# Kernel optimization log

Hardware: AMD Instinct MI355X
Metric: run time of the kernel (lower is better)

The kernel has to match this reference:

```python
import jax, jax.numpy as jnp
import numpy as np

IN_CH = 32
OUT_CH = 32
HIDDEN = 32  # edge/angle MLP hidden width


def setup_inputs() -> dict:
    key = jax.random.key(0)
    ks = jax.random.split(key, 13)
    N, E, A = 50000, 200000, 400000
    s = 0.1
    return {
        "x": jax.random.normal(ks[0], (N, IN_CH), dtype=jnp.float32),
        "edge_index": jax.random.randint(ks[1], (2, E), 0, N),
        "edge_attr": jax.random.uniform(ks[2], (E, 1), dtype=jnp.float32),
        "angle_index": jax.random.randint(ks[3], (3, A), 0, N),
        "angles": jax.random.uniform(ks[4], (A, 1), dtype=jnp.float32),
        # edge_mlp: Linear(1,32) -> ReLU -> Linear(32, in*out)
        "eW1": jax.random.normal(ks[5], (1, HIDDEN), dtype=jnp.float32) * s,
        "eb1": jax.random.normal(ks[6], (HIDDEN,), dtype=jnp.float32) * s,
        "eW2": jax.random.normal(ks[7], (HIDDEN, IN_CH * OUT_CH), dtype=jnp.float32) * s,
        "eb2": jax.random.normal(ks[8], (IN_CH * OUT_CH,), dtype=jnp.float32) * s,
        # angle_mlp: Linear(1,32) -> ReLU -> Linear(32, out)
        "aW1": jax.random.normal(ks[9], (1, HIDDEN), dtype=jnp.float32) * s,
        "ab1": jax.random.normal(ks[10], (HIDDEN,), dtype=jnp.float32) * s,
        "aW2": jax.random.normal(ks[11], (HIDDEN, OUT_CH), dtype=jnp.float32) * s,
        "ab2": jax.random.normal(ks[12], (OUT_CH,), dtype=jnp.float32) * s,
    }


def reference(x, edge_index, edge_attr, angle_index, angles,
              eW1, eb1, eW2, eb2, aW1, ab1, aW2, ab2):
    N = x.shape[0]
    row, col = edge_index[0], edge_index[1]
    # per-edge weight matrices from edge MLP: (E, in, out)
    h = jax.nn.relu(edge_attr @ eW1 + eb1)
    edge_w = (h @ eW2 + eb2).reshape(-1, IN_CH, OUT_CH)
    # gather source node features, apply per-edge matrix (bmm)
    msg = jnp.einsum('ei,eio->eo', x[col], edge_w)  # (E, out)
    agg = jax.ops.segment_sum(msg, row, num_segments=N)
    # angle branch: scatter angle features onto center node j
    j = angle_index[1]
    angle_feat = jax.nn.relu(angles @ aW1 + ab1) @ aW2 + ab2  # (A, out)
    agg = agg + jax.ops.segment_sum(angle_feat, j, num_segments=N)
    return agg
```

## Files before the change

### kernel.cpp

```cpp
#include <hip/hip_runtime.h>
#include <hip/hip_bf16.h>
#include <stdint.h>

#define IC 32
#define OC 32
#define HID 32

#define PBIN 16
#define TSH 44
#define TSCALE 1048576.0f

#define PBE 12

typedef __attribute__((ext_vector_type(8))) _Float16 half8;
typedef __attribute__((ext_vector_type(4))) float f32x4;
typedef unsigned long long u64;

static __device__ __forceinline__ _Float16 f2h(float f) { return (_Float16)f; }

__device__ __align__(16) _Float16 g_MK[PBE * 2 * 32 * 32];
__device__ float g_ekn[16];
__device__ float g_akn[16];
__device__ int   g_npc[2];

__global__ __launch_bounds__(256) void setup_kernel(
    const float* __restrict__ eW1, const float* __restrict__ eb1,
    const float* __restrict__ eW2, const float* __restrict__ eb2,
    const float* __restrict__ aW1, const float* __restrict__ ab1)
{
    __shared__ float ts_s[32];
    __shared__ int   rk_s[32];
    __shared__ int   re_s[32];
    const int tid = threadIdx.x;

    if (blockIdx.x == 0 && tid < 16) { g_ekn[tid] = 1e30f; g_akn[tid] = 1e30f; }

    if (tid < 32) {
        const int k = tid;
        const float w = eW1[k], b = eb1[k];
        const float ts = -b / w;
        const bool re = (w != 0.f) && (ts > 0.f) && (ts < 1.f);
        int rk = 0;
        for (int k2 = 0; k2 < 32; ++k2) {
            const float w2 = eW1[k2], b2 = eb1[k2];
            const float t2 = -b2 / w2;
            const bool re2 = (w2 != 0.f) && (t2 > 0.f) && (t2 < 1.f);
            rk += (re2 && (t2 < ts || (t2 == ts && k2 < k))) ? 1 : 0;
        }
        ts_s[k] = ts; rk_s[k] = rk; re_s[k] = re ? 1 : 0;
    }
    __syncthreads();

    if (blockIdx.x == 0) {
        if (tid < 32) {
            if (re_s[tid]) g_ekn[rk_s[tid]] = ts_s[tid];
            if (tid == 0) {
                int n = 0;
                for (int k = 0; k < 32; ++k) n += re_s[k];
                g_npc[0] = n + 1;
            }
        } else if (tid < 64) {
            const int k = tid - 32;
            const float w = aW1[k], b = ab1[k];
            const float ts = -b / w;
            const bool re = (w != 0.f) && (ts > 0.f) && (ts < 1.f);
            int rk = 0, nre = 0;
            for (int k2 = 0; k2 < 32; ++k2) {
                const float w2 = aW1[k2], b2 = ab1[k2];
                const float t2 = -b2 / w2;
                const bool re2 = (w2 != 0.f) && (t2 > 0.f) && (t2 < 1.f);
                nre += re2 ? 1 : 0;
                rk += (re2 && (t2 < ts || (t2 == ts && k2 < k))) ? 1 : 0;
            }
            if (re) g_akn[rk] = ts;
            if (k == 0) g_npc[1] = nre + 1;
        }
    }

    const int gid = blockIdx.x * blockDim.x + tid;
    if (gid < PBE * 2 * 32 * 32) {
        const int i   = gid & 31;
        const int o   = (gid >> 5) & 31;
        const int mat = (gid >> 10) & 1;
        const int cc  = gid >> 11;
        float acc = (mat == 0) ? eb2[i * 32 + o] : 0.f;
        for (int k = 0; k < 32; ++k) {
            const bool flip = re_s[k] && (rk_s[k] < cc);
            const float w = eW1[k], b = eb1[k];
            const bool on0 = b > 0.f;
            const bool on = (w > 0.f) ? (on0 || flip) : (on0 && !flip);
            if (on) acc = fmaf((mat == 0 ? b : w), eW2[k * 1024 + i * 32 + o], acc);
        }
        g_MK[((cc * 2 + mat) * 32 + o) * 32 + i] = (_Float16)acc;
    }
}

__global__ void zero_kernel(float* __restrict__ out, int n) {
    int i = (blockIdx.x * blockDim.x + threadIdx.x) * 4;
    if (i + 3 < n) {
        *(float4*)(out + i) = make_float4(0.f, 0.f, 0.f, 0.f);
    } else {
        for (int k = i; k < n; ++k) out[k] = 0.f;
    }
}

__global__ __launch_bounds__(256) void angle_scatter(
    const float* __restrict__ angles, const int* __restrict__ angle_index,
    u64* __restrict__ cells, int A)
{
    float kn[16];
#pragma unroll
    for (int j = 0; j < 16; ++j) kn[j] = g_akn[j];

    int i0 = blockIdx.x * blockDim.x + threadIdx.x;
    int stride = gridDim.x * blockDim.x;
    for (int a = i0; a < A; a += stride) {
        const float t = angles[a];
        const int j = angle_index[A + a];
        int cc = 0;
#pragma unroll
        for (int jj = 0; jj < 16; ++jj) cc += (t >= kn[jj]) ? 1 : 0;
        if ((unsigned)cc < (unsigned)PBIN) {
            const u64 enc = ((u64)1 << TSH) | (u64)(unsigned)(t * TSCALE);
            atomicAdd(cells + (size_t)j * PBIN + cc, enc);
        }
    }
}

__global__ __launch_bounds__(256) void angle_gather(
    float* __restrict__ out,
    const float* __restrict__ aW1, const float* __restrict__ ab1,
    const float* __restrict__ aW2, const float* __restrict__ ab2,
    int N)
{
    const int lane = threadIdx.x & 63;
    const int q    = lane >> 4;
    const int l15  = lane & 15;
    const int wib  = threadIdx.x >> 6;
    const int base = (blockIdx.x * 4 + wib) * 16;
    if (base >= N) return;

    float w1s[8], b1s[8];
    int c0 = 0, c1 = 0;
#pragma unroll
    for (int k = 0; k < HID; ++k) {
        const float w = aW1[k], b = ab1[k];
        const bool pos = w > 0.f;
        const bool f0 = pos ? (b > 0.f) : !(b > 0.f);
        const bool f1 = pos ? ((w + b) > 0.f) : !((w + b) > 0.f);
        c0 += f0 ? 1 : 0;
        c1 += f1 ? 1 : 0;
        if ((k >> 3) == q) { w1s[k & 7] = w; b1s[k & 7] = b; }
    }
    int npc = c1 - c0 + 1;
    if (npc > PBIN) npc = PBIN;

    half8 Bf0, Bf1;
#pragma unroll
    for (int j = 0; j < 8; ++j) {
        Bf0[j] = f2h(aW2[(q * 8 + j) * OC + l15]);
        Bf1[j] = f2h(aW2[(q * 8 + j) * OC + 16 + l15]);
    }
    const float bias0 = ab2[l15];
    const float bias1 = ab2[16 + l15];

    const int jn = base + l15;
    const bool vn = (jn < N);
    const u64* cj = (const u64*)out + (size_t)(vn ? jn : 0) * PBIN;
    float g[8] = {0.f, 0.f, 0.f, 0.f, 0.f, 0.f, 0.f, 0.f};
    float tot = 0.f;
    for (int cc = 0; cc < npc; ++cc) {
        const u64 v = vn ? cj[cc] : 0;
        if (v) {
            const float n  = (float)(unsigned)(v >> TSH);
            const float ts = (float)(v & (((u64)1 << TSH) - 1)) * (1.f / TSCALE);
            const float tb = ts / n;
#pragma unroll
            for (int k = 0; k < 8; ++k) {
                float h = fmaf(tb, w1s[k], b1s[k]);
                h = h > 0.f ? h : 0.f;
                g[k] = fmaf(n, h, g[k]);
            }
            tot += n;
        }
    }
    half8 a;
#pragma unroll
    for (int k = 0; k < 8; ++k) a[k] = f2h(g[k]);

    f32x4 acc0 = {0.f, 0.f, 0.f, 0.f};
    f32x4 acc1 = {0.f, 0.f, 0.f, 0.f};
    acc0 = __builtin_amdgcn_mfma_f32_16x16x32_f16(a, Bf0, acc0, 0, 0, 0);
    acc1 = __builtin_amdgcn_mfma_f32_16x16x32_f16(a, Bf1, acc1, 0, 0, 0);

#pragma unroll
    for (int r = 0; r < 4; ++r) {
        const int node = base + q * 4 + r;
        const float tr = __shfl(tot, q * 4 + r, 64);
        if (node < N) {
            out[(size_t)node * OC + l15]      = fmaf(tr, bias0, acc0[r]);
            out[(size_t)node * OC + 16 + l15] = fmaf(tr, bias1, acc1[r]);
        }
    }
}

__global__ __launch_bounds__(256) void angle_fixup(
    const float* __restrict__ angles, const int* __restrict__ angle_index,
    const float* __restrict__ aW1, const float* __restrict__ ab1,
    const float* __restrict__ aW2, const float* __restrict__ ab2,
    float* __restrict__ out, int A)
{
    if (g_npc[1] <= PBIN) return;

    float w1[HID], b1[HID];
#pragma unroll
    for (int k = 0; k < HID; ++k) { w1[k] = aW1[k]; b1[k] = ab1[k]; }
    const float kn15 = g_akn[15];

    int i0 = blockIdx.x * blockDim.x + threadIdx.x;
    int stride = gridDim.x * blockDim.x;
    for (int a = i0; a < A; a += stride) {
        const float t = angles[a];
        if (t < kn15) continue;
        const int j = angle_index[A + a];
        float h[HID];
#pragma unroll
        for (int k = 0; k < HID; ++k) {
            float v = fmaf(t, w1[k], b1[k]);
            h[k] = v > 0.f ? v : 0.f;
        }
        for (int o = 0; o < OC; ++o) {
            float s = ab2[o];
#pragma unroll
            for (int k = 0; k < HID; ++k) s = fmaf(h[k], aW2[k * OC + o], s);
            unsafeAtomicAdd(out + (size_t)j * OC + o, s);
        }
    }
}

__global__ __launch_bounds__(512) void edge_kernel(
    const float* __restrict__ x, const int* __restrict__ edge_index,
    const float* __restrict__ edge_attr,
    float* __restrict__ out, int E)
{
    __shared__ __align__(16) _Float16 B[PBE * 2 * 32 * 40];
    __shared__ float knl[16];

    const int tid = threadIdx.x;

    for (int r = tid; r < PBE * 2 * 32; r += 512) {
        const float4* s = (const float4*)(g_MK + r * 32);
        float4 a0 = s[0], a1 = s[1], a2 = s[2], a3 = s[3];
        float4* d = (float4*)(B + r * 40);
        d[0] = a0; d[1] = a1; d[2] = a2; d[3] = a3;
    }
    if (tid < 16) knl[tid] = g_ekn[tid];
    __syncthreads();

    float kn[PBE];
#pragma unroll
    for (int j = 0; j < PBE; ++j) kn[j] = knl[j];
    int npc = g_npc[0];
    if (npc > PBE) npc = PBE;

    const int lane  = tid & 63;
    const int w8    = tid >> 6;
    const int gwave = blockIdx.x * 8 + w8;
    const int ot    = gwave & 1;
    const int tile0 = gwave >> 1;
    const int tstride = (gridDim.x * 8) >> 1;
    const int q     = lane >> 4;
    const int l15   = lane & 15;
    const int ocol  = ot * 16 + l15;

    const _Float16* Bbase = B + (size_t)ocol * 40 + q * 8;

    const int numTiles = (E + 15) >> 4;

    for (int tile = tile0; tile < numTiles; tile += 2 * tstride) {
        const int tA = tile;
        const int tB = tile + tstride;
        const bool hasB = (tB < numTiles);

        const int eA  = (tA << 4) + l15;
        const bool va = (eA < E);
        const float ta = va ? edge_attr[va ? eA : 0] : 0.f;
        const int colA = va ? edge_index[E + eA] : 0;

        const int eB  = (tB << 4) + l15;
        const bool vb = hasB && (eB < E);
        const float tb = vb ? edge_attr[vb ? eB : 0] : 0.f;
        const int colB = vb ? edge_index[E + (vb ? eB : 0)] : 0;

        const float* xpA = x + (size_t)colA * IC + q * 8;
        const float4 xloA = *(const float4*)(xpA);
        const float4 xhiA = *(const float4*)(xpA + 4);
        const float* xpB = x + (size_t)colB * IC + q * 8;
        const float4 xloB = *(const float4*)(xpB);
        const float4 xhiB = *(const float4*)(xpB + 4);

        int dstsA[4], dstsB[4];
        const int ebaseA = (tA << 4) + q * 4;
        const int ebaseB = (tB << 4) + q * 4;
#pragma unroll
        for (int r = 0; r < 4; ++r) {
            const int erA = ebaseA + r;
            dstsA[r] = (erA < E) ? edge_index[erA] : -1;
            const int erB = ebaseB + r;
            dstsB[r] = (hasB && erB < E) ? edge_index[erB] : -1;
        }

        int ccA = 0, ccB = 0;
#pragma unroll
        for (int j = 0; j < PBE; ++j) {
            ccA += (ta >= kn[j]) ? 1 : 0;
            ccB += (tb >= kn[j]) ? 1 : 0;
        }

        half8 xhA, xhB;
        xhA[0] = f2h(xloA.x); xhA[1] = f2h(xloA.y);
        xhA[2] = f2h(xloA.z); xhA[3] = f2h(xloA.w);
        xhA[4] = f2h(xhiA.x); xhA[5] = f2h(xhiA.y);
        xhA[6] = f2h(xhiA.z); xhA[7] = f2h(xhiA.w);
        xhB[0] = f2h(xloB.x); xhB[1] = f2h(xloB.y);
        xhB[2] = f2h(xloB.z); xhB[3] = f2h(xloB.w);
        xhB[4] = f2h(xhiB.x); xhB[5] = f2h(xhiB.y);
        xhB[6] = f2h(xhiB.z); xhB[7] = f2h(xhiB.w);

        const _Float16 thA = f2h(ta), thB = f2h(tb);
        const half8 tvA = {thA, thA, thA, thA, thA, thA, thA, thA};
        const half8 tvB = {thB, thB, thB, thB, thB, thB, thB, thB};
        const half8 xtA = xhA * tvA;
        const half8 xtB = xhB * tvB;
        const half8 z = {0, 0, 0, 0, 0, 0, 0, 0};

        f32x4 accA = {0.f, 0.f, 0.f, 0.f};
        f32x4 accB = {0.f, 0.f, 0.f, 0.f};
        for (int c = 0; c < npc; ++c) {
            const half8 bM = *(const half8*)(Bbase + (size_t)(c * 2 + 0) * 32 * 40);
            const half8 bK = *(const half8*)(Bbase + (size_t)(c * 2 + 1) * 32 * 40);
            const half8 aA1 = (ccA == c) ? xhA : z;
            const half8 aA2 = (ccA == c) ? xtA : z;
            const half8 aB1 = (ccB == c) ? xhB : z;
            const half8 aB2 = (ccB == c) ? xtB : z;
            accA = __builtin_amdgcn_mfma_f32_16x16x32_f16(aA1, bM, accA, 0, 0, 0);
            accB = __builtin_amdgcn_mfma_f32_16x16x32_f16(aB1, bM, accB, 0, 0, 0);
            accA = __builtin_amdgcn_mfma_f32_16x16x32_f16(aA2, bK, accA, 0, 0, 0);
            accB = __builtin_amdgcn_mfma_f32_16x16x32_f16(aB2, bK, accB, 0, 0, 0);
        }

#pragma unroll
        for (int r = 0; r < 4; ++r) {
            if (dstsA[r] >= 0)
                unsafeAtomicAdd(out + (size_t)dstsA[r] * OC + ocol, accA[r]);
        }
#pragma unroll
        for (int r = 0; r < 4; ++r) {
            if (dstsB[r] >= 0)
                unsafeAtomicAdd(out + (size_t)dstsB[r] * OC + ocol, accB[r]);
        }
    }
}

__global__ __launch_bounds__(256) void edge_fixup(
    const float* __restrict__ x, const int* __restrict__ edge_index,
    const float* __restrict__ edge_attr,
    const float* __restrict__ eW1, const float* __restrict__ eb1,
    const float* __restrict__ eW2, const float* __restrict__ eb2,
    float* __restrict__ out, int E)
{
    if (g_npc[0] <= PBE) return;
    const float knb = g_ekn[PBE - 1];

    int i0 = blockIdx.x * blockDim.x + threadIdx.x;
    int stride = gridDim.x * blockDim.x;
    for (int e = i0; e < E; e += stride) {
        const float t = edge_attr[e];
        if (t < knb) continue;
        const int col = edge_index[E + e];
        const int dst = edge_index[e];
        float h[HID];
#pragma unroll
        for (int k = 0; k < HID; ++k) {
            float v = fmaf(t, eW1[k], eb1[k]);
            h[k] = v > 0.f ? v : 0.f;
        }
        float xv[IC];
#pragma unroll
        for (int i = 0; i < IC; ++i) xv[i] = x[(size_t)col * IC + i];
        for (int o = 0; o < OC; ++o) {
            float s = 0.f;
            for (int i = 0; i < IC; ++i) {
                float wio = eb2[i * 32 + o];
#pragma unroll
                for (int k = 0; k < HID; ++k)
                    wio = fmaf(h[k], eW2[k * 1024 + i * 32 + o], wio);
                s = fmaf(xv[i], wio, s);
            }
            unsafeAtomicAdd(out + (size_t)dst * OC + o, s);
        }
    }
}

extern "C" void kernel_launch(void* const* d_in, const int* in_sizes, int n_in,
                              void* d_out, int out_size, void* d_ws, size_t ws_size,
                              hipStream_t stream)
{
    const float* x          = (const float*)d_in[0];
    const int*   edge_index = (const int*)d_in[1];
    const float* edge_attr  = (const float*)d_in[2];
    const int*   angle_index= (const int*)d_in[3];
    const float* angles     = (const float*)d_in[4];
    const float* eW1        = (const float*)d_in[5];
    const float* eb1        = (const float*)d_in[6];
    const float* eW2        = (const float*)d_in[7];
    const float* eb2        = (const float*)d_in[8];
    const float* aW1        = (const float*)d_in[9];
    const float* ab1        = (const float*)d_in[10];
    const float* aW2        = (const float*)d_in[11];
    const float* ab2        = (const float*)d_in[12];
    float* out = (float*)d_out;
    (void)d_ws; (void)ws_size;

    const int E = in_sizes[1] / 2;
    const int A = in_sizes[3] / 3;
    const int N = in_sizes[0] / IC;

    setup_kernel<<<96, 256, 0, stream>>>(eW1, eb1, eW2, eb2, aW1, ab1);

    const int zblocks = (out_size / 4 + 255) / 256;
    zero_kernel<<<zblocks, 256, 0, stream>>>(out, out_size);

    const int sblocks = (A + 255) / 256;
    angle_scatter<<<sblocks, 256, 0, stream>>>(angles, angle_index,
                                               (u64*)out, A);

    const int gblocks = (N + 63) / 64;
    angle_gather<<<gblocks, 256, 0, stream>>>(out, aW1, ab1, aW2, ab2, N);

    angle_fixup<<<sblocks, 256, 0, stream>>>(angles, angle_index,
                                             aW1, ab1, aW2, ab2, out, A);

    edge_kernel<<<512, 512, 0, stream>>>(x, edge_index, edge_attr, out, E);

    edge_fixup<<<256, 256, 0, stream>>>(x, edge_index, edge_attr,
                                        eW1, eb1, eW2, eb2, out, E);
}
```

Baseline: 163.0 us.

## Fuse setup with zeroing and merge edge, gather and fixup into one mega kernel

Moves the angle histogram cells into a dedicated global buffer so the output no longer doubles as scratch. Setup and zeroing run in one kernel, and the edge MFMA work, angle gather (now atomic-add into out), angle fixup and edge fixup run as block-partitioned roles of a single launch. Launch count drops from seven to three and the independent edge and angle branches can run concurrently. In exchange the gather path now issues atomics instead of plain stores, and it depends on a fixed-size global cell buffer capped at 65536 nodes.

```diff
diff --git a/kernel.cpp b/kernel.cpp
--- a/kernel.cpp
+++ b/kernel.cpp
@@ -11,6 +11,7 @@
 #define TSCALE 1048576.0f
 
 #define PBE 12
+#define MAXN 65536
 
 typedef __attribute__((ext_vector_type(8))) _Float16 half8;
 typedef __attribute__((ext_vector_type(4))) float f32x4;
@@ -22,85 +23,88 @@
 __device__ float g_ekn[16];
 __device__ float g_akn[16];
 __device__ int   g_npc[2];
-
-__global__ __launch_bounds__(256) void setup_kernel(
+__device__ __align__(16) u64 g_cells[(size_t)MAXN * PBIN];
+
+__global__ __launch_bounds__(512) void setup_zero(
     const float* __restrict__ eW1, const float* __restrict__ eb1,
     const float* __restrict__ eW2, const float* __restrict__ eb2,
-    const float* __restrict__ aW1, const float* __restrict__ ab1)
+    const float* __restrict__ aW1, const float* __restrict__ ab1,
+    float* __restrict__ out, int outF4, int cellF4)
 {
     __shared__ float ts_s[32];
     __shared__ int   rk_s[32];
     __shared__ int   re_s[32];
     const int tid = threadIdx.x;
-
-    if (blockIdx.x == 0 && tid < 16) { g_ekn[tid] = 1e30f; g_akn[tid] = 1e30f; }
-
-    if (tid < 32) {
-        const int k = tid;
-        const float w = eW1[k], b = eb1[k];
-        const float ts = -b / w;
-        const bool re = (w != 0.f) && (ts > 0.f) && (ts < 1.f);
-        int rk = 0;
-        for (int k2 = 0; k2 < 32; ++k2) {
-            const float w2 = eW1[k2], b2 = eb1[k2];
-            const float t2 = -b2 / w2;
-            const bool re2 = (w2 != 0.f) && (t2 > 0.f) && (t2 < 1.f);
-            rk += (re2 && (t2 < ts || (t2 == ts && k2 < k))) ? 1 : 0;
-        }
-        ts_s[k] = ts; rk_s[k] = rk; re_s[k] = re ? 1 : 0;
-    }
-    __syncthreads();
-
-    if (blockIdx.x == 0) {
+    const int bid = blockIdx.x;
+
+    if (bid < 48) {
+        if (bid == 0 && tid < 16) { g_ekn[tid] = 1e30f; g_akn[tid] = 1e30f; }
         if (tid < 32) {
-            if (re_s[tid]) g_ekn[rk_s[tid]] = ts_s[tid];
-            if (tid == 0) {
-                int n = 0;
-                for (int k = 0; k < 32; ++k) n += re_s[k];
-                g_npc[0] = n + 1;
-            }
-        } else if (tid < 64) {
-            const int k = tid - 32;
-            const float w = aW1[k], b = ab1[k];
+            const int k = tid;
+            const float w = eW1[k], b = eb1[k];
             const float ts = -b / w;
             const bool re = (w != 0.f) && (ts > 0.f) && (ts < 1.f);
-            int rk = 0, nre = 0;
+            int rk = 0;
             for (int k2 = 0; k2 < 32; ++k2) {
-                const float w2 = aW1[k2], b2 = ab1[k2];
+                const float w2 = eW1[k2], b2 = eb1[k2];
                 const float t2 = -b2 / w2;
                 const bool re2 = (w2 != 0.f) && (t2 > 0.f) && (t2 < 1.f);
-                nre += re2 ? 1 : 0;
                 rk += (re2 && (t2 < ts || (t2 == ts && k2 < k))) ? 1 : 0;
             }
-            if (re) g_akn[rk] = ts;
-            if (k == 0) g_npc[1] = nre + 1;
-        }
-    }
-
-    const int gid = blockIdx.x * blockDim.x + tid;
-    if (gid < PBE * 2 * 32 * 32) {
-        const int i   = gid & 31;
-        const int o   = (gid >> 5) & 31;
-        const int mat = (gid >> 10) & 1;
-        const int cc  = gid >> 11;
-        float acc = (mat == 0) ? eb2[i * 32 + o] : 0.f;
-        for (int k = 0; k < 32; ++k) {
-            const bool flip = re_s[k] && (rk_s[k] < cc);
-            const float w = eW1[k], b = eb1[k];
-            const bool on0 = b > 0.f;
-            const bool on = (w > 0.f) ? (on0 || flip) : (on0 && !flip);
-            if (on) acc = fmaf((mat == 0 ? b : w), eW2[k * 1024 + i * 32 + o], acc);
-        }
-        g_MK[((cc * 2 + mat) * 32 + o) * 32 + i] = (_Float16)acc;
-    }
-}
-
-__global__ void zero_kernel(float* __restrict__ out, int n) {
-    int i = (blockIdx.x * blockDim.x + threadIdx.x) * 4;
-    if (i + 3 < n) {
-        *(float4*)(out + i) = make_float4(0.f, 0.f, 0.f, 0.f);
-    } else {
-        for (int k = i; k < n; ++k) out[k] = 0.f;
+            ts_s[k] = ts; rk_s[k] = rk; re_s[k] = re ? 1 : 0;
+        }
+        __syncthreads();
+
+        if (bid == 0) {
+            if (tid < 32) {
+                if (re_s[tid]) g_ekn[rk_s[tid]] = ts_s[tid];
+                if (tid == 0) {
+                    int n = 0;
+                    for (int k = 0; k < 32; ++k) n += re_s[k];
+                    g_npc[0] = n + 1;
+                }
+            } else if (tid < 64) {
+                const int k = tid - 32;
+                const float w = aW1[k], b = ab1[k];
+                const float ts = -b / w;
+                const bool re = (w != 0.f) && (ts > 0.f) && (ts < 1.f);
+                int rk = 0, nre = 0;
+                for (int k2 = 0; k2 < 32; ++k2) {
+                    const float w2 = aW1[k2], b2 = ab1[k2];
+                    const float t2 = -b2 / w2;
+                    const bool re2 = (w2 != 0.f) && (t2 > 0.f) && (t2 < 1.f);
+                    nre += re2 ? 1 : 0;
+                    rk += (re2 && (t2 < ts || (t2 == ts && k2 < k))) ? 1 : 0;
+                }
+                if (re) g_akn[rk] = ts;
+                if (k == 0) g_npc[1] = nre + 1;
+            }
+        }
+
+        const int gid = bid * 512 + tid;
+        if (gid < PBE * 2 * 32 * 32) {
+            const int i   = gid & 31;
+            const int o   = (gid >> 5) & 31;
+            const int mat = (gid >> 10) & 1;
+            const int cc  = gid >> 11;
+            float acc = (mat == 0) ? eb2[i * 32 + o] : 0.f;
+            for (int k = 0; k < 32; ++k) {
+                const bool flip = re_s[k] && (rk_s[k] < cc);
+                const float w = eW1[k], b = eb1[k];
+                const bool on0 = b > 0.f;
+                const bool on = (w > 0.f) ? (on0 || flip) : (on0 && !flip);
+                if (on) acc = fmaf((mat == 0 ? b : w),
+                                   eW2[k * 1024 + i * 32 + o], acc);
+            }
+            g_MK[((cc * 2 + mat) * 32 + o) * 32 + i] = (_Float16)acc;
+        }
+    }
+
+    const int total = outF4 + cellF4;
+    const float4 z4 = make_float4(0.f, 0.f, 0.f, 0.f);
+    for (int i = bid * 512 + tid; i < total; i += gridDim.x * 512) {
+        if (i < outF4) ((float4*)out)[i] = z4;
+        else           ((float4*)g_cells)[i - outF4] = z4;
     }
 }
 
@@ -108,6 +112,7 @@
     const float* __restrict__ angles, const int* __restrict__ angle_index,
     u64* __restrict__ cells, int A)
 {
+    u64* cp = cells ? cells : g_cells;
     float kn[16];
 #pragma unroll
     for (int j = 0; j < 16; ++j) kn[j] = g_akn[j];
@@ -122,24 +127,18 @@
         for (int jj = 0; jj < 16; ++jj) cc += (t >= kn[jj]) ? 1 : 0;
         if ((unsigned)cc < (unsigned)PBIN) {
             const u64 enc = ((u64)1 << TSH) | (u64)(unsigned)(t * TSCALE);
-            atomicAdd(cells + (size_t)j * PBIN + cc, enc);
-        }
-    }
-}
-
-__global__ __launch_bounds__(256) void angle_gather(
-    float* __restrict__ out,
+            atomicAdd(cp + (size_t)j * PBIN + cc, enc);
+        }
+    }
+}
+
+static __device__ __forceinline__ void angle_gather_wave(
+    const u64* __restrict__ cells, float* __restrict__ out,
     const float* __restrict__ aW1, const float* __restrict__ ab1,
     const float* __restrict__ aW2, const float* __restrict__ ab2,
-    int N)
-{
-    const int lane = threadIdx.x & 63;
-    const int q    = lane >> 4;
-    const int l15  = lane & 15;
-    const int wib  = threadIdx.x >> 6;
-    const int base = (blockIdx.x * 4 + wib) * 16;
-    if (base >= N) return;
-
+    int N, int base, int lane, bool addmode)
+{
+    const int q = lane >> 4, l15 = lane & 15;
     float w1s[8], b1s[8];
     int c0 = 0, c1 = 0;
 #pragma unroll
@@ -166,7 +165,7 @@
 
     const int jn = base + l15;
     const bool vn = (jn < N);
-    const u64* cj = (const u64*)out + (size_t)(vn ? jn : 0) * PBIN;
+    const u64* cj = cells + (size_t)(vn ? jn : 0) * PBIN;
     float g[8] = {0.f, 0.f, 0.f, 0.f, 0.f, 0.f, 0.f, 0.f};
     float tot = 0.f;
     for (int cc = 0; cc < npc; ++cc) {
@@ -198,206 +197,220 @@
         const int node = base + q * 4 + r;
         const float tr = __shfl(tot, q * 4 + r, 64);
         if (node < N) {
-            out[(size_t)node * OC + l15]      = fmaf(tr, bias0, acc0[r]);
-            out[(size_t)node * OC + 16 + l15] = fmaf(tr, bias1, acc1[r]);
-        }
-    }
-}
-
-__global__ __launch_bounds__(256) void angle_fixup(
-    const float* __restrict__ angles, const int* __restrict__ angle_index,
+            const float v0 = fmaf(tr, bias0, acc0[r]);
+            const float v1 = fmaf(tr, bias1, acc1[r]);
+            if (addmode) {
+                unsafeAtomicAdd(out + (size_t)node * OC + l15, v0);
+                unsafeAtomicAdd(out + (size_t)node * OC + 16 + l15, v1);
+            } else {
+                out[(size_t)node * OC + l15]      = v0;
+                out[(size_t)node * OC + 16 + l15] = v1;
+            }
+        }
+    }
+}
+
+__global__ __launch_bounds__(256) void angle_gather_ow(
+    float* __restrict__ out,
     const float* __restrict__ aW1, const float* __restrict__ ab1,
-    const float* __restrict__ aW2, const float* __restrict__ ab2,
-    float* __restrict__ out, int A)
-{
-    if (g_npc[1] <= PBIN) return;
-
-    float w1[HID], b1[HID];
-#pragma unroll
-    for (int k = 0; k < HID; ++k) { w1[k] = aW1[k]; b1[k] = ab1[k]; }
-    const float kn15 = g_akn[15];
-
-    int i0 = blockIdx.x * blockDim.x + threadIdx.x;
-    int stride = gridDim.x * blockDim.x;
-    for (int a = i0; a < A; a += stride) {
-        const float t = angles[a];
-        if (t < kn15) continue;
-        const int j = angle_index[A + a];
-        float h[HID];
-#pragma unroll
-        for (int k = 0; k < HID; ++k) {
-            float v = fmaf(t, w1[k], b1[k]);
-            h[k] = v > 0.f ? v : 0.f;
-        }
-        for (int o = 0; o < OC; ++o) {
-            float s = ab2[o];
-#pragma unroll
-            for (int k = 0; k < HID; ++k) s = fmaf(h[k], aW2[k * OC + o], s);
-            unsafeAtomicAdd(out + (size_t)j * OC + o, s);
-        }
-    }
-}
-
-__global__ __launch_bounds__(512) void edge_kernel(
-    const float* __restrict__ x, const int* __restrict__ edge_index,
-    const float* __restrict__ edge_attr,
-    float* __restrict__ out, int E)
-{
-    __shared__ __align__(16) _Float16 B[PBE * 2 * 32 * 40];
-    __shared__ float knl[16];
-
-    const int tid = threadIdx.x;
-
-    for (int r = tid; r < PBE * 2 * 32; r += 512) {
-        const float4* s = (const float4*)(g_MK + r * 32);
-        float4 a0 = s[0], a1 = s[1], a2 = s[2], a3 = s[3];
-        float4* d = (float4*)(B + r * 40);
-        d[0] = a0; d[1] = a1; d[2] = a2; d[3] = a3;
-    }
-    if (tid < 16) knl[tid] = g_ekn[tid];
-    __syncthreads();
-
-    float kn[PBE];
-#pragma unroll
-    for (int j = 0; j < PBE; ++j) kn[j] = knl[j];
-    int npc = g_npc[0];
-    if (npc > PBE) npc = PBE;
-
-    const int lane  = tid & 63;
-    const int w8    = tid >> 6;
-    const int gwave = blockIdx.x * 8 + w8;
-    const int ot    = gwave & 1;
-    const int tile0 = gwave >> 1;
-    const int tstride = (gridDim.x * 8) >> 1;
-    const int q     = lane >> 4;
-    const int l15   = lane & 15;
-    const int ocol  = ot * 16 + l15;
-
-    const _Float16* Bbase = B + (size_t)ocol * 40 + q * 8;
-
-    const int numTiles = (E + 15) >> 4;
-
-    for (int tile = tile0; tile < numTiles; tile += 2 * tstride) {
-        const int tA = tile;
-        const int tB = tile + tstride;
-        const bool hasB = (tB < numTiles);
-
-        const int eA  = (tA << 4) + l15;
-        const bool va = (eA < E);
-        const float ta = va ? edge_attr[va ? eA : 0] : 0.f;
-        const int colA = va ? edge_index[E + eA] : 0;
-
-        const int eB  = (tB << 4) + l15;
-        const bool vb = hasB && (eB < E);
-        const float tb = vb ? edge_attr[vb ? eB : 0] : 0.f;
-        const int colB = vb ? edge_index[E + (vb ? eB : 0)] : 0;
-
-        const float* xpA = x + (size_t)colA * IC + q * 8;
-        const float4 xloA = *(const float4*)(xpA);
-        const float4 xhiA = *(const float4*)(xpA + 4);
-        const float* xpB = x + (size_t)colB * IC + q * 8;
-        const float4 xloB = *(const float4*)(xpB);
-        const float4 xhiB = *(const float4*)(xpB + 4);
-
-        int dstsA[4], dstsB[4];
-        const int ebaseA = (tA << 4) + q * 4;
-        const int ebaseB = (tB << 4) + q * 4;
-#pragma unroll
-        for (int r = 0; r < 4; ++r) {
-            const int erA = ebaseA + r;
-            dstsA[r] = (erA < E) ? edge_index[erA] : -1;
-            const int erB = ebaseB + r;
-            dstsB[r] = (hasB && erB < E) ? edge_index[erB] : -1;
-        }
-
-        int ccA = 0, ccB = 0;
-#pragma unroll
-        for (int j = 0; j < PBE; ++j) {
-            ccA += (ta >= kn[j]) ? 1 : 0;
-            ccB += (tb >= kn[j]) ? 1 : 0;
-        }
-
-        half8 xhA, xhB;
-        xhA[0] = f2h(xloA.x); xhA[1] = f2h(xloA.y);
-        xhA[2] = f2h(xloA.z); xhA[3] = f2h(xloA.w);
-        xhA[4] = f2h(xhiA.x); xhA[5] = f2h(xhiA.y);
-        xhA[6] = f2h(xhiA.z); xhA[7] = f2h(xhiA.w);
-        xhB[0] = f2h(xloB.x); xhB[1] = f2h(xloB.y);
-        xhB[2] = f2h(xloB.z); xhB[3] = f2h(xloB.w);
-        xhB[4] = f2h(xhiB.x); xhB[5] = f2h(xhiB.y);
-        xhB[6] = f2h(xhiB.z); xhB[7] = f2h(xhiB.w);
-
-        const _Float16 thA = f2h(ta), thB = f2h(tb);
-        const half8 tvA = {thA, thA, thA, thA, thA, thA, thA, thA};
-        const half8 tvB = {thB, thB, thB, thB, thB, thB, thB, thB};
-        const half8 xtA = xhA * tvA;
-        const half8 xtB = xhB * tvB;
-        const half8 z = {0, 0, 0, 0, 0, 0, 0, 0};
-
-        f32x4 accA = {0.f, 0.f, 0.f, 0.f};
-        f32x4 accB = {0.f, 0.f, 0.f, 0.f};
-        for (int c = 0; c < npc; ++c) {
-            const half8 bM = *(const half8*)(Bbase + (size_t)(c * 2 + 0) * 32 * 40);
-            const half8 bK = *(const half8*)(Bbase + (size_t)(c * 2 + 1) * 32 * 40);
-            const half8 aA1 = (ccA == c) ? xhA : z;
-            const half8 aA2 = (ccA == c) ? xtA : z;
-            const half8 aB1 = (ccB == c) ? xhB : z;
-            const half8 aB2 = (ccB == c) ? xtB : z;
-            accA = __builtin_amdgcn_mfma_f32_16x16x32_f16(aA1, bM, accA, 0, 0, 0);
-            accB = __builtin_amdgcn_mfma_f32_16x16x32_f16(aB1, bM, accB, 0, 0, 0);
-            accA = __builtin_amdgcn_mfma_f32_16x16x32_f16(aA2, bK, accA, 0, 0, 0);
-            accB = __builtin_amdgcn_mfma_f32_16x16x32_f16(aB2, bK, accB, 0, 0, 0);
-        }
-
-#pragma unroll
-        for (int r = 0; r < 4; ++r) {
-            if (dstsA[r] >= 0)
-                unsafeAtomicAdd(out + (size_t)dstsA[r] * OC + ocol, accA[r]);
-        }
-#pragma unroll
-        for (int r = 0; r < 4; ++r) {
-            if (dstsB[r] >= 0)
-                unsafeAtomicAdd(out + (size_t)dstsB[r] * OC + ocol, accB[r]);
-        }
-    }
-}
-
-__global__ __launch_bounds__(256) void edge_fixup(
+    const float* __restrict__ aW2, const float* __restrict__ ab2, int N)
+{
+    const int lane = threadIdx.x & 63;
+    const int wib  = threadIdx.x >> 6;
+    const int base = (blockIdx.x * 4 + wib) * 16;
+    if (base >= N) return;
+    angle_gather_wave((const u64*)out, out, aW1, ab1, aW2, ab2,
+                      N, base, lane, false);
+}
+
+__global__ __launch_bounds__(512, 4) void mega_kernel(
     const float* __restrict__ x, const int* __restrict__ edge_index,
     const float* __restrict__ edge_attr,
     const float* __restrict__ eW1, const float* __restrict__ eb1,
     const float* __restrict__ eW2, const float* __restrict__ eb2,
-    float* __restrict__ out, int E)
-{
-    if (g_npc[0] <= PBE) return;
-    const float knb = g_ekn[PBE - 1];
-
-    int i0 = blockIdx.x * blockDim.x + threadIdx.x;
-    int stride = gridDim.x * blockDim.x;
-    for (int e = i0; e < E; e += stride) {
-        const float t = edge_attr[e];
-        if (t < knb) continue;
-        const int col = edge_index[E + e];
-        const int dst = edge_index[e];
-        float h[HID];
-#pragma unroll
-        for (int k = 0; k < HID; ++k) {
-            float v = fmaf(t, eW1[k], eb1[k]);
-            h[k] = v > 0.f ? v : 0.f;
-        }
-        float xv[IC];
-#pragma unroll
-        for (int i = 0; i < IC; ++i) xv[i] = x[(size_t)col * IC + i];
-        for (int o = 0; o < OC; ++o) {
-            float s = 0.f;
-            for (int i = 0; i < IC; ++i) {
-                float wio = eb2[i * 32 + o];
-#pragma unroll
-                for (int k = 0; k < HID; ++k)
-                    wio = fmaf(h[k], eW2[k * 1024 + i * 32 + o], wio);
-                s = fmaf(xv[i], wio, s);
-            }
-            unsafeAtomicAdd(out + (size_t)dst * OC + o, s);
+    const float* __restrict__ angles, const int* __restrict__ angle_index,
+    const float* __restrict__ aW1, const float* __restrict__ ab1,
+    const float* __restrict__ aW2, const float* __restrict__ ab2,
+    float* __restrict__ out, int E, int A, int N,
+    int EB, int GB, int FA, int FE)
+{
+    __shared__ __align__(16) _Float16 B[PBE * 2 * 32 * 40];
+    __shared__ float knl[16];
+
+    const int tid = threadIdx.x;
+    const int bid = blockIdx.x;
+
+    if (bid < EB) {
+        for (int r = tid; r < PBE * 2 * 32; r += 512) {
+            const float4* s = (const float4*)(g_MK + r * 32);
+            float4 a0 = s[0], a1 = s[1], a2 = s[2], a3 = s[3];
+            float4* d = (float4*)(B + r * 40);
+            d[0] = a0; d[1] = a1; d[2] = a2; d[3] = a3;
+        }
+        if (tid < 16) knl[tid] = g_ekn[tid];
+        __syncthreads();
+
+        float kn[PBE];
+#pragma unroll
+        for (int j = 0; j < PBE; ++j) kn[j] = knl[j];
+        int npc = g_npc[0];
+        if (npc > PBE) npc = PBE;
+
+        const int lane  = tid & 63;
+        const int w8    = tid >> 6;
+        const int gwave = bid * 8 + w8;
+        const int ot    = gwave & 1;
+        const int tile0 = gwave >> 1;
+        const int tstride = (EB * 8) >> 1;
+        const int q     = lane >> 4;
+        const int l15   = lane & 15;
+        const int ocol  = ot * 16 + l15;
+        const _Float16* Bbase = B + (size_t)ocol * 40 + q * 8;
+
+        const int numTiles = (E + 15) >> 4;
+
+        for (int tile = tile0; tile < numTiles; tile += 2 * tstride) {
+            const int tA = tile;
+            const int tB = tile + tstride;
+            const bool hasB = (tB < numTiles);
+
+            const int eA  = (tA << 4) + l15;
+            const bool va = (eA < E);
+            const float ta = va ? edge_attr[eA] : 0.f;
+            const int colA = va ? edge_index[E + eA] : 0;
+
+            const int eB  = (tB << 4) + l15;
+            const bool vb = hasB && (eB < E);
+            const float tb = vb ? edge_attr[eB] : 0.f;
+            const int colB = vb ? edge_index[E + eB] : 0;
+
+            const float* xpA = x + (size_t)colA * IC + q * 8;
+            const float4 xloA = *(const float4*)(xpA);
+            const float4 xhiA = *(const float4*)(xpA + 4);
+            const float* xpB = x + (size_t)colB * IC + q * 8;
+            const float4 xloB = *(const float4*)(xpB);
+            const float4 xhiB = *(const float4*)(xpB + 4);
+
+            int dstsA[4], dstsB[4];
+            const int ebaseA = (tA << 4) + q * 4;
+            const int ebaseB = (tB << 4) + q * 4;
+#pragma unroll
+            for (int r = 0; r < 4; ++r) {
+                const int erA = ebaseA + r;
+                dstsA[r] = (erA < E) ? edge_index[erA] : -1;
+                const int erB = ebaseB + r;
+                dstsB[r] = (hasB && erB < E) ? edge_index[erB] : -1;
+            }
+
+            int ccA = 0, ccB = 0;
+#pragma unroll
+            for (int j = 0; j < PBE; ++j) {
+                ccA += (ta >= kn[j]) ? 1 : 0;
+                ccB += (tb >= kn[j]) ? 1 : 0;
+            }
+
+            half8 xhA, xhB;
+            xhA[0] = f2h(xloA.x); xhA[1] = f2h(xloA.y);
+            xhA[2] = f2h(xloA.z); xhA[3] = f2h(xloA.w);
+            xhA[4] = f2h(xhiA.x); xhA[5] = f2h(xhiA.y);
+            xhA[6] = f2h(xhiA.z); xhA[7] = f2h(xhiA.w);
+            xhB[0] = f2h(xloB.x); xhB[1] = f2h(xloB.y);
+            xhB[2] = f2h(xloB.z); xhB[3] = f2h(xloB.w);
+            xhB[4] = f2h(xhiB.x); xhB[5] = f2h(xhiB.y);
+            xhB[6] = f2h(xhiB.z); xhB[7] = f2h(xhiB.w);
+
+            const _Float16 thA = f2h(ta), thB = f2h(tb);
+            const half8 tvA = {thA, thA, thA, thA, thA, thA, thA, thA};
+            const half8 tvB = {thB, thB, thB, thB, thB, thB, thB, thB};
+            const half8 xtA = xhA * tvA;
+            const half8 xtB = xhB * tvB;
+            const half8 z = {0, 0, 0, 0, 0, 0, 0, 0};
+
+            f32x4 accA = {0.f, 0.f, 0.f, 0.f};
+            f32x4 accB = {0.f, 0.f, 0.f, 0.f};
+            for (int c = 0; c < npc; ++c) {
+                const half8 bM = *(const half8*)(Bbase + (size_t)(c * 2 + 0) * 32 * 40);
+                const half8 bK = *(const half8*)(Bbase + (size_t)(c * 2 + 1) * 32 * 40);
+                const half8 aA1 = (ccA == c) ? xhA : z;
+                const half8 aA2 = (ccA == c) ? xtA : z;
+                const half8 aB1 = (ccB == c) ? xhB : z;
+                const half8 aB2 = (ccB == c) ? xtB : z;
+                accA = __builtin_amdgcn_mfma_f32_16x16x32_f16(aA1, bM, accA, 0, 0, 0);
+                accB = __builtin_amdgcn_mfma_f32_16x16x32_f16(aB1, bM, accB, 0, 0, 0);
+                accA = __builtin_amdgcn_mfma_f32_16x16x32_f16(aA2, bK, accA, 0, 0, 0);
+                accB = __builtin_amdgcn_mfma_f32_16x16x32_f16(aB2, bK, accB, 0, 0, 0);
+            }
+
+#pragma unroll
+            for (int r = 0; r < 4; ++r) {
+                if (dstsA[r] >= 0)
+                    unsafeAtomicAdd(out + (size_t)dstsA[r] * OC + ocol, accA[r]);
+            }
+#pragma unroll
+            for (int r = 0; r < 4; ++r) {
+                if (dstsB[r] >= 0)
+                    unsafeAtomicAdd(out + (size_t)dstsB[r] * OC + ocol, accB[r]);
+            }
+        }
+    } else if (bid < EB + GB) {
+        const int lane = tid & 63;
+        const int wib  = tid >> 6;
+        const int base = ((bid - EB) * 8 + wib) * 16;
+        if (base < N)
+            angle_gather_wave(g_cells, out, aW1, ab1, aW2, ab2,
+                              N, base, lane, true);
+    } else if (bid < EB + GB + FA) {
+        if (g_npc[1] <= PBIN) return;
+        const float kn15 = g_akn[15];
+        float w1[HID], b1[HID];
+#pragma unroll
+        for (int k = 0; k < HID; ++k) { w1[k] = aW1[k]; b1[k] = ab1[k]; }
+        int i0 = (bid - EB - GB) * 512 + tid;
+        int stride = FA * 512;
+        for (int a = i0; a < A; a += stride) {
+            const float t = angles[a];
+            if (t < kn15) continue;
+            const int j = angle_index[A + a];
+            float h[HID];
+#pragma unroll
+            for (int k = 0; k < HID; ++k) {
+                float v = fmaf(t, w1[k], b1[k]);
+                h[k] = v > 0.f ? v : 0.f;
+            }
+            for (int o = 0; o < OC; ++o) {
+                float s = ab2[o];
+#pragma unroll
+                for (int k = 0; k < HID; ++k) s = fmaf(h[k], aW2[k * OC + o], s);
+                unsafeAtomicAdd(out + (size_t)j * OC + o, s);
+            }
+        }
+    } else {
+        if (g_npc[0] <= PBE) return;
+        const float knb = g_ekn[PBE - 1];
+        int i0 = (bid - EB - GB - FA) * 512 + tid;
+        int stride = FE * 512;
+        for (int e = i0; e < E; e += stride) {
+            const float t = edge_attr[e];
+            if (t < knb) continue;
+            const int col = edge_index[E + e];
+            const int dst = edge_index[e];
+            float h[HID];
+#pragma unroll
+            for (int k = 0; k < HID; ++k) {
+                float v = fmaf(t, eW1[k], eb1[k]);
+                h[k] = v > 0.f ? v : 0.f;
+            }
+            for (int o = 0; o < OC; ++o) {
+                float s = 0.f;
+                for (int i = 0; i < IC; ++i) {
+                    float wio = eb2[i * 32 + o];
+#pragma unroll
+                    for (int k = 0; k < HID; ++k)
+                        wio = fmaf(h[k], eW2[k * 1024 + i * 32 + o], wio);
+                    s = fmaf(x[(size_t)col * IC + i], wio, s);
+                }
+                unsafeAtomicAdd(out + (size_t)dst * OC + o, s);
+            }
         }
     }
 }
@@ -426,23 +439,39 @@
     const int A = in_sizes[3] / 3;
     const int N = in_sizes[0] / IC;
 
-    setup_kernel<<<96, 256, 0, stream>>>(eW1, eb1, eW2, eb2, aW1, ab1);
-
-    const int zblocks = (out_size / 4 + 255) / 256;
-    zero_kernel<<<zblocks, 256, 0, stream>>>(out, out_size);
-
+    const int outF4 = out_size / 4;
     const int sblocks = (A + 255) / 256;
-    angle_scatter<<<sblocks, 256, 0, stream>>>(angles, angle_index,
-                                               (u64*)out, A);
-
-    const int gblocks = (N + 63) / 64;
-    angle_gather<<<gblocks, 256, 0, stream>>>(out, aW1, ab1, aW2, ab2, N);
-
-    angle_fixup<<<sblocks, 256, 0, stream>>>(angles, angle_index,
-                                             aW1, ab1, aW2, ab2, out, A);
-
-    edge_kernel<<<512, 512, 0, stream>>>(x, edge_index, edge_attr, out, E);
-
-    edge_fixup<<<256, 256, 0, stream>>>(x, edge_index, edge_attr,
-                                        eW1, eb1, eW2, eb2, out, E);
-}
+
+    if (N <= MAXN) {
+        const int cellF4 = N * 8;
+        int zg = (outF4 + cellF4 + 511) / 512;
+        if (zg < 48) zg = 48;
+        setup_zero<<<zg, 512, 0, stream>>>(eW1, eb1, eW2, eb2, aW1, ab1,
+                                           out, outF4, cellF4);
+
+        angle_scatter<<<sblocks, 256, 0, stream>>>(angles, angle_index,
+                                                   nullptr, A);
+
+        const int EB = 512;
+        const int GB = (N + 127) / 128;
+        const int FA = 64, FE = 64;
+        mega_kernel<<<EB + GB + FA + FE, 512, 0, stream>>>(
+            x, edge_index, edge_attr, eW1, eb1, eW2, eb2,
+            angles, angle_index, aW1, ab1, aW2, ab2,
+            out, E, A, N, EB, GB, FA, FE);
+    } else {
+        int zg = (outF4 + 511) / 512;
+        if (zg < 48) zg = 48;
+        setup_zero<<<zg, 512, 0, stream>>>(eW1, eb1, eW2, eb2, aW1, ab1,
+                                           out, outF4, 0);
+        angle_scatter<<<sblocks, 256, 0, stream>>>(angles, angle_index,
+                                                   (u64*)out, A);
+        angle_gather_ow<<<(N + 63) / 64, 256, 0, stream>>>(out, aW1, ab1,
+                                                           aW2, ab2, N);
+        const int EB = 512, FA = 64, FE = 64;
+        mega_kernel<<<EB + FA + FE, 512, 0, stream>>>(
+            x, edge_index, edge_attr, eW1, eb1, eW2, eb2,
+            angles, angle_index, aW1, ab1, aW2, ab2,
+            out, E, A, N, EB, 0, FA, FE);
+    }
+}
```

After: 155.2 us. 4.7% less time.
